# Optimization experiments

Measured on AMD Instinct MI355X. Metric: run time of the kernel, lower is better.

Reference implementation:

```python
import jax, jax.numpy as jnp
import numpy as np

DIM, STATE, EXPAND = 1024, 16, 2
INNER = DIM * EXPAND  # 2048
KSIZE = 4
BATCH, SEQ = 2, 2048


def setup_inputs() -> dict:
    key = jax.random.key(0)
    ks = jax.random.split(key, 7)
    s = 0.02
    return {
        "x": jax.random.normal(ks[0], (BATCH, SEQ, DIM), jnp.float32),
        "W_in": jax.random.normal(ks[1], (2 * INNER, DIM), jnp.float32) * s,
        "conv_w": jax.random.normal(ks[2], (INNER, 1, KSIZE), jnp.float32) * s,
        "conv_b": jnp.zeros((INNER,), jnp.float32),
        "W_x": jax.random.normal(ks[3], (2 * STATE + 1, INNER), jnp.float32) * s,
        "W_dt": jax.random.normal(ks[4], (INNER, STATE), jnp.float32) * s,
        "b_dt": jnp.zeros((INNER,), jnp.float32),
        "W_out": jax.random.normal(ks[5], (DIM, INNER), jnp.float32) * s,
        "A_log": jnp.log(jnp.broadcast_to(
            jnp.arange(1, STATE + 1, dtype=jnp.float32), (INNER, STATE))),
    }


def reference(x, W_in, conv_w, conv_b, W_x, W_dt, b_dt, W_out, A_log):
    b, n, _ = x.shape
    xr = x @ W_in.T                                  # [b,n,2*inner]
    u, res = jnp.split(xr, 2, axis=-1)               # each [b,n,inner]

    # Depthwise conv1d. Original uses padding=3 on both sides but the scan
    # loop only consumes the first n timesteps, which equals a causal conv
    # with left padding KSIZE-1.
    uc = jnp.transpose(u, (0, 2, 1))                 # [b,inner,n]
    uc = jax.lax.conv_general_dilated(
        uc, conv_w, window_strides=(1,), padding=[(KSIZE - 1, 0)],
        dimension_numbers=("NCH", "OIH", "NCH"), feature_group_count=INNER)
    u = jnp.transpose(uc + conv_b[None, :, None], (0, 2, 1))  # [b,n,inner]

    ssm = u @ W_x.T                                  # [b,n,2*state+1]
    dt_in = ssm[..., :STATE]                         # [b,n,state]
    B = ssm[..., STATE:2 * STATE]                    # [b,n,state]
    C = ssm[..., -1]                                 # [b,n]  (scalar readout per step)
    delta = jax.nn.softplus(dt_in @ W_dt.T + b_dt)   # [b,n,inner]
    A = -jnp.exp(A_log)                              # [inner,state]

    def step(h, ts):
        d_t, u_t, b_t, c_t = ts                      # [b,inner],[b,inner],[b,state],[b]
        h = h * jnp.exp(d_t[:, :, None] * A) + u_t[:, :, None] * b_t[:, None, :]
        y = jnp.sum(h, axis=-1) * c_t[:, None]       # y = (h @ C), C scalar
        return h, y

    h0 = jnp.zeros((b, INNER, STATE), x.dtype)
    xs = (jnp.moveaxis(delta, 1, 0), jnp.moveaxis(u, 1, 0),
          jnp.moveaxis(B, 1, 0), jnp.moveaxis(C, 1, 0))
    _, ys = jax.lax.scan(step, h0, xs)               # ys: [n,b,inner]
    y = jnp.moveaxis(ys, 0, 1)                       # [b,n,inner]

    y = y * jax.nn.silu(res)
    return y @ W_out.T                               # [b,n,dim]
```

## Files before the change

### kernel.cpp

```cpp
#include <hip/hip_runtime.h>
#include <math.h>

#define SEQL   2048
#define DIMM   1024
#define NST    16
#define INR    2048
#define TOKS   4096
#define LCH    256
#define NCH    8
#define WARM   64

typedef _Float16 f16;
typedef _Float16 f16x8 __attribute__((ext_vector_type(8)));
typedef float    f32x4 __attribute__((ext_vector_type(4)));

__device__ __forceinline__ int swz(int r) { return (r & 3) ^ ((r >> 2) & 3); }

#define GLDS(SRC, DST) __builtin_amdgcn_global_load_lds( \
    (const __attribute__((address_space(1))) void*)(SRC), \
    (__attribute__((address_space(3))) void*)(DST), 16, 0, 0)

__device__ __forceinline__ void cvt8hi(const float* __restrict__ in, int i,
                                       f16* __restrict__ hi)
{
    const float4* p = (const float4*)(in + (size_t)i * 8);
    float4 a = p[0], b = p[1];
    float v[8] = {a.x, a.y, a.z, a.w, b.x, b.y, b.z, b.w};
    f16x8 H;
    #pragma unroll
    for (int j = 0; j < 8; ++j) H[j] = (f16)v[j];
    *(f16x8*)(hi + (size_t)i * 8) = H;
}

__global__ __launch_bounds__(256) void k_prep(
        const float* __restrict__ Wx,   float* __restrict__ WxT,
        const float* __restrict__ x,    f16* __restrict__ Xhi,
        const float* __restrict__ Win,  f16* __restrict__ Whi,
        const float* __restrict__ Wout, f16* __restrict__ WoH)
{
    const int b = blockIdx.x, tid = threadIdx.x;
    if (b < 264) {
        int i = b * 256 + tid;
        int j = i / INR, ch = i % INR;
        WxT[ch * 33 + j] = Wx[i];
    } else if (b < 264 + 2048) {
        cvt8hi(x, (b - 264) * 256 + tid, Xhi);
    } else if (b < 264 + 4096) {
        cvt8hi(Win, (b - 264 - 2048) * 256 + tid, Whi);
    } else {
        cvt8hi(Wout, (b - 264 - 4096) * 256 + tid, WoH);
    }
}

template<int BN>
__global__ __launch_bounds__(256, 4) void k_gemm(
        const f16* __restrict__ Ah, const f16* __restrict__ Bh,
        int Kloop, int Kstride, int epi, int Nst,
        float* __restrict__ out0, float* __restrict__ out1)
{
    __shared__ alignas(16) f16 SM[8192 + BN * 64];

    const int tid = threadIdx.x;
    const int l   = tid & 63;
    const int w   = tid >> 6;
    const int wm  = (w >> 1) * 64;
    const int wn  = (w & 1) * (BN / 2);
    const int lr  = l & 15;
    const int kg  = l >> 4;
    const int NF  = BN / 32;

    const int wg = blockIdx.x, xcd = wg & 7, pos = wg >> 3;
    int bx, by, kz;
    if (epi) {
        by = (xcd >> 2) * 16 + (pos >> 3);
        bx = (xcd & 3) * 8 + (pos & 7);
        kz = 0;
    } else {
        kz = xcd >> 2;
        by = pos >> 2;
        bx = (xcd & 3) * 4 + (pos & 3);
    }
    const int m0 = by * 128;
    const int n0 = bx * BN;
    const int koff = kz * Kloop;

    const int srow = l >> 2;
    const int sc   = (l & 3) ^ swz(srow);
    const int fo   = lr * 32 + (kg ^ swz(lr)) * 8;

    f32x4 acc[4][4];
    #pragma unroll
    for (int mi = 0; mi < 4; ++mi)
        #pragma unroll
        for (int ni = 0; ni < NF; ++ni)
            acc[mi][ni] = (f32x4){0.f, 0.f, 0.f, 0.f};

    for (int k0 = 0; k0 < Kloop; k0 += 64) {
        __syncthreads();
        #pragma unroll
        for (int hh = 0; hh < 2; ++hh) {
            #pragma unroll
            for (int q = 0; q < 2; ++q) {
                const int rl = w * 32 + q * 16 + srow;
                const size_t go =
                    (size_t)(m0 + rl) * Kstride + koff + k0 + hh * 32 + sc * 8;
                GLDS(Ah + go, &SM[hh * 4096 + (w * 32 + q * 16) * 32]);
            }
            #pragma unroll
            for (int q = 0; q < BN / 64; ++q) {
                const int rl = w * (BN / 4) + q * 16 + srow;
                const size_t go =
                    (size_t)(n0 + rl) * Kstride + koff + k0 + hh * 32 + sc * 8;
                GLDS(Bh + go,
                     &SM[8192 + hh * (BN * 32) + (w * (BN / 4) + q * 16) * 32]);
            }
        }
        __syncthreads();

        #pragma unroll
        for (int hh = 0; hh < 2; ++hh) {
            f16x8 a_[4], b_[4];
            #pragma unroll
            for (int mi = 0; mi < 4; ++mi)
                a_[mi] = *(const f16x8*)&SM[hh * 4096 + (wm + mi * 16) * 32 + fo];
            #pragma unroll
            for (int ni = 0; ni < NF; ++ni)
                b_[ni] = *(const f16x8*)
                    &SM[8192 + hh * (BN * 32) + (wn + ni * 16) * 32 + fo];
            #pragma unroll
            for (int mi = 0; mi < 4; ++mi)
                #pragma unroll
                for (int ni = 0; ni < NF; ++ni)
                    acc[mi][ni] = __builtin_amdgcn_mfma_f32_16x16x32_f16(
                                      a_[mi], b_[ni], acc[mi][ni], 0, 0, 0);
        }
    }

    const int r0 = (l >> 4) * 4;
    float* dst0 = out0 + (epi ? 0 : (size_t)kz * 4194304);
    #pragma unroll
    for (int mi = 0; mi < 4; ++mi)
        #pragma unroll
        for (int ni = 0; ni < NF; ++ni) {
            const int col = n0 + wn + ni * 16 + (l & 15);
            #pragma unroll
            for (int rr = 0; rr < 4; ++rr) {
                const int row = m0 + wm + mi * 16 + r0 + rr;
                float v = acc[mi][ni][rr];
                if (epi) {
                    if (col < INR) {
                        out0[(size_t)row * INR + col] = v;
                    } else {
                        float s = v / (1.f + __expf(-v));
                        out1[(size_t)row * INR + (col - INR)] = s;
                    }
                } else {
                    dst0[(size_t)row * Nst + col] = v;
                }
            }
        }
}

__global__ __launch_bounds__(256) void k_addout(const float* __restrict__ p,
                                                float* __restrict__ out)
{
    int i = blockIdx.x * 256 + threadIdx.x;
    float4 a = ((const float4*)p)[i];
    float4 b = ((const float4*)(p + 4194304))[i];
    float4 o = {a.x + b.x, a.y + b.y, a.z + b.z, a.w + b.w};
    ((float4*)out)[i] = o;
}

__global__ __launch_bounds__(256) void k_conv(const float* __restrict__ u0,
        const float* __restrict__ cw, const float* __restrict__ cb,
        float* __restrict__ uct)
{
    __shared__ float S[67][65];
    const int tid = threadIdx.x;
    const int ch0 = blockIdx.x * 64;
    const int t0  = blockIdx.y * 64;
    const int b   = blockIdx.z;
    const int ci  = tid & 63;
    for (int r = tid >> 6; r < 67; r += 4) {
        int t = t0 - 3 + r;
        S[r][ci] = (t < 0) ? 0.f : u0[((size_t)b*SEQL + t)*INR + ch0 + ci];
    }
    __syncthreads();
    const int ti = tid & 63;
    const int cq = tid >> 6;
    #pragma unroll
    for (int q = 0; q < 16; ++q) {
        int c  = cq + q*4;
        int ch = ch0 + c;
        float w0 = cw[ch*4+0], w1 = cw[ch*4+1], w2 = cw[ch*4+2], w3 = cw[ch*4+3];
        float acc = cb[ch]
            + w0*S[ti+0][c] + w1*S[ti+1][c] + w2*S[ti+2][c] + w3*S[ti+3][c];
        uct[((size_t)b*INR + ch)*SEQL + t0 + ti] = acc;
    }
}

__global__ __launch_bounds__(256) void k_ssm_part(const float* __restrict__ uct,
        const float* __restrict__ WxT, float* __restrict__ part)
{
    const int t  = blockIdx.x * 256 + threadIdx.x;
    const int cs = blockIdx.y;
    const int b  = blockIdx.z;
    const int ch0 = cs * 64;
    float acc[33];
    #pragma unroll
    for (int j = 0; j < 33; ++j) acc[j] = 0.f;
    const float* up = uct + ((size_t)b*INR + ch0)*SEQL + t;
    for (int c = 0; c < 64; ++c) {
        float uv = up[(size_t)c * SEQL];
        const float* wr = WxT + (size_t)(ch0 + c) * 33;
        #pragma unroll
        for (int j = 0; j < 33; ++j) acc[j] = fmaf(uv, wr[j], acc[j]);
    }
    #pragma unroll
    for (int j = 0; j < 33; ++j)
        part[(((size_t)j*32 + cs)*2 + b)*SEQL + t] = acc[j];
}

__global__ __launch_bounds__(256) void k_ssm_reduce(const float* __restrict__ part,
        float* __restrict__ dtin, float* __restrict__ Bm, float* __restrict__ Cv)
{
    int g = blockIdx.x * 256 + threadIdx.x;
    if (g >= 33 * TOKS) return;
    int j = g / TOKS, m = g % TOKS;
    int b = m >> 11, t = m & 2047;
    float s = 0.f;
    #pragma unroll
    for (int cs = 0; cs < 32; ++cs)
        s += part[(((size_t)j*32 + cs)*2 + b)*SEQL + t];
    if (j < 16)      dtin[m*16 + j] = s;
    else if (j < 32) Bm[m*16 + (j-16)] = s;
    else             Cv[m] = s;
}

__global__ __launch_bounds__(256) void k_delta(const float* __restrict__ dtin,
        const float* __restrict__ Wdt, const float* __restrict__ bdt,
        float* __restrict__ dT)
{
    __shared__ float Ds[16][68];
    __shared__ float Ws[16][68];
    const int tid = threadIdx.x;
    const int c0 = blockIdx.x * 64;
    const int m0 = blockIdx.y * 64;
    const int r = tid >> 2, kq = (tid & 3) * 4;
    {
        float4 dv = *(const float4*)&dtin[(size_t)(m0 + r)*16 + kq];
        float4 wv = *(const float4*)&Wdt [(size_t)(c0 + r)*16 + kq];
        Ds[kq+0][r]=dv.x; Ds[kq+1][r]=dv.y; Ds[kq+2][r]=dv.z; Ds[kq+3][r]=dv.w;
        Ws[kq+0][r]=wv.x; Ws[kq+1][r]=wv.y; Ws[kq+2][r]=wv.z; Ws[kq+3][r]=wv.w;
    }
    __syncthreads();
    const int tx = tid & 15, ty = tid >> 4;
    float acc[4][4];
    #pragma unroll
    for (int i = 0; i < 4; ++i)
        #pragma unroll
        for (int j = 0; j < 4; ++j) acc[i][j] = 0.f;
    #pragma unroll
    for (int kk = 0; kk < 16; ++kk) {
        float4 a4 = *(const float4*)&Ds[kk][ty*4];
        float4 b4 = *(const float4*)&Ws[kk][tx*4];
        float a[4] = {a4.x, a4.y, a4.z, a4.w};
        float wv[4] = {b4.x, b4.y, b4.z, b4.w};
        #pragma unroll
        for (int i = 0; i < 4; ++i)
            #pragma unroll
            for (int j = 0; j < 4; ++j)
                acc[i][j] = fmaf(a[i], wv[j], acc[i][j]);
    }
    const int b = m0 >> 11;
    const int tbase = (m0 & 2047) + ty*4;
    #pragma unroll
    for (int j = 0; j < 4; ++j) {
        int ch = c0 + tx*4 + j;
        float bias = bdt[ch];
        float4 o;
        o.x = log1pf(__expf(acc[0][j] + bias));
        o.y = log1pf(__expf(acc[1][j] + bias));
        o.z = log1pf(__expf(acc[2][j] + bias));
        o.w = log1pf(__expf(acc[3][j] + bias));
        *(float4*)&dT[((size_t)b*INR + ch)*SEQL + tbase] = o;
    }
}

__global__ __launch_bounds__(256) void k_scan(const float* __restrict__ dT,
        const float* __restrict__ uct, const float* __restrict__ Bm,
        const float* __restrict__ Cv, const float* __restrict__ Alog,
        const float* __restrict__ sres, f16* __restrict__ AoH)
{
    __shared__ float dS[16][68];
    __shared__ float uS[16][68];
    __shared__ float bT[16][68];
    __shared__ float cS[64];
    __shared__ float hS[16*272];
    const int tid = threadIdx.x;
    const int g = tid >> 4, s = tid & 15;
    const int ch0 = blockIdx.x * 16;
    const int c   = blockIdx.y;
    const int b   = blockIdx.z;
    const int ch  = ch0 + g;
    const int tbase = c * LCH;
    const size_t mb = (size_t)b * SEQL;
    const float A = -__expf(Alog[ch*NST + s]);
    float h = 0.f;
    const int row = tid >> 4, col4 = (tid & 15) * 4;
    const int sB = tid & 15, tq = tid >> 4;
    const int ci = tid & 15, tw = tid >> 4;
    const float* dRow = dT  + ((size_t)b*INR + ch0 + row)*SEQL + tbase;
    const float* uRow = uct + ((size_t)b*INR + ch0 + row)*SEQL + tbase;

    for (int t0 = (c ? -WARM : 0); t0 < LCH; t0 += 64) {
        __syncthreads();
        *(float4*)&dS[row][col4] = *(const float4*)&dRow[t0 + col4];
        *(float4*)&uS[row][col4] = *(const float4*)&uRow[t0 + col4];
        #pragma unroll
        for (int k = 0; k < 4; ++k)
            bT[sB][tq*4 + k] = Bm[(mb + tbase + t0 + tq*4 + k)*16 + sB];
        if (t0 >= 0 && tid < 64) cS[tid] = Cv[mb + tbase + t0 + tid];
        __syncthreads();
        if (t0 < 0) {
            #pragma unroll
            for (int q = 0; q < 16; ++q) {
                float4 d4 = *(const float4*)&dS[g][q*4];
                float4 u4 = *(const float4*)&uS[g][q*4];
                float4 b4 = *(const float4*)&bT[s][q*4];
                h = fmaf(h, __expf(d4.x*A), u4.x*b4.x);
                h = fmaf(h, __expf(d4.y*A), u4.y*b4.y);
                h = fmaf(h, __expf(d4.z*A), u4.z*b4.z);
                h = fmaf(h, __expf(d4.w*A), u4.w*b4.w);
            }
            continue;
        }
        #pragma unroll
        for (int sub = 0; sub < 4; ++sub) {
            #pragma unroll
            for (int q = 0; q < 4; ++q) {
                float4 d4 = *(const float4*)&dS[g][sub*16 + q*4];
                float4 u4 = *(const float4*)&uS[g][sub*16 + q*4];
                float4 b4 = *(const float4*)&bT[s][sub*16 + q*4];
                h = fmaf(h, __expf(d4.x*A), u4.x*b4.x);
                hS[(q*4+0)*272 + g*17 + s] = h;
                h = fmaf(h, __expf(d4.y*A), u4.y*b4.y);
                hS[(q*4+1)*272 + g*17 + s] = h;
                h = fmaf(h, __expf(d4.z*A), u4.z*b4.z);
                hS[(q*4+2)*272 + g*17 + s] = h;
                h = fmaf(h, __expf(d4.w*A), u4.w*b4.w);
                hS[(q*4+3)*272 + g*17 + s] = h;
            }
            __syncthreads();
            float v = 0.f;
            #pragma unroll
            for (int ss = 0; ss < 16; ++ss)
                v += hS[tw*272 + ci*17 + ss];
            const int tl = sub*16 + tw;
            const size_t gi = (mb + tbase + t0 + tl)*INR + ch0 + ci;
            AoH[gi] = (f16)((v * cS[tl]) * sres[gi]);
            __syncthreads();
        }
    }
}

extern "C" void kernel_launch(void* const* d_in, const int* in_sizes, int n_in,
                              void* d_out, int out_size, void* d_ws, size_t ws_size,
                              hipStream_t stream)
{
    (void)in_sizes; (void)n_in; (void)out_size; (void)ws_size;
    const float* x     = (const float*)d_in[0];
    const float* W_in  = (const float*)d_in[1];
    const float* cw    = (const float*)d_in[2];
    const float* cb    = (const float*)d_in[3];
    const float* W_x   = (const float*)d_in[4];
    const float* W_dt  = (const float*)d_in[5];
    const float* b_dt  = (const float*)d_in[6];
    const float* W_out = (const float*)d_in[7];
    const float* A_log = (const float*)d_in[8];
    float* out = (float*)d_out;

    float* ws = (float*)d_ws;
    const size_t MI = 1024 * 1024;
    float* u0   = ws;
    float* sres = ws + 8*MI;
    float* uct  = ws + 16*MI;
    float* part = ws + 24*MI;
    float* dtin = ws + 32*MI;
    float* Bm   = dtin + 65536;
    float* Cv   = Bm + 65536;
    float* WxT  = Cv + 4096;
    float* dT   = u0;
    f16* Xhi = (f16*)(ws + 16*MI);
    f16* Whi = (f16*)(ws + 18*MI);
    f16* AoH = (f16*)(ws + 24*MI);
    f16* WoH = (f16*)(ws + 30*MI);
    float* pK = sres;

    k_prep     <<<dim3(264 + 2048 + 2048 + 1024), 256, 0, stream>>>(
                    W_x, WxT, x, Xhi, W_in, Whi, W_out, WoH);
    k_gemm<128><<<dim3(1024), 256, 0, stream>>>(Xhi, Whi,
                    DIMM, DIMM, 1, INR, u0, sres);
    k_conv     <<<dim3(32, 32, 2), 256, 0, stream>>>(u0, cw, cb, uct);
    k_ssm_part <<<dim3(8, 32, 2), 256, 0, stream>>>(uct, WxT, part);
    k_ssm_reduce<<<dim3((33*TOKS + 255)/256), 256, 0, stream>>>(part, dtin, Bm, Cv);
    k_delta    <<<dim3(32, 64), 256, 0, stream>>>(dtin, W_dt, b_dt, dT);
    k_scan     <<<dim3(128, NCH, 2), 256, 0, stream>>>(dT, uct, Bm, Cv, A_log,
                    sres, AoH);
    k_gemm<64> <<<dim3(1024), 256, 0, stream>>>(AoH, WoH,
                    DIMM, INR, 0, DIMM, pK, nullptr);
    k_addout   <<<dim3(4096), 256, 0, stream>>>(pK, out);
}
```

Baseline: 225.3 us.

## Store conv output and scan partial states in fp16; widen output GEMM tile

The depthwise conv output is stored as fp16 instead of fp32, which halves the traffic for the SSM projection and scan kernels that read it. The scan's shared-memory state buffer becomes fp16, reducing LDS footprint. Separately, the output projection GEMM switches to a 128-wide N tile with half the workgroups and a remapped block index. The cost is lower precision in u and in the partial-state sums.

```diff
diff --git a/kernel.cpp b/kernel.cpp
--- a/kernel.cpp
+++ b/kernel.cpp
@@ -12,6 +12,7 @@
 
 typedef _Float16 f16;
 typedef _Float16 f16x8 __attribute__((ext_vector_type(8)));
+typedef _Float16 f16x4v __attribute__((ext_vector_type(4)));
 typedef float    f32x4 __attribute__((ext_vector_type(4)));
 
 __device__ __forceinline__ int swz(int r) { return (r & 3) ^ ((r >> 2) & 3); }
@@ -77,8 +78,8 @@
         kz = 0;
     } else {
         kz = xcd >> 2;
-        by = pos >> 2;
-        bx = (xcd & 3) * 4 + (pos & 3);
+        by = pos >> 1;
+        bx = (xcd & 3) * 2 + (pos & 1);
     }
     const int m0 = by * 128;
     const int n0 = bx * BN;
@@ -173,7 +174,7 @@
 
 __global__ __launch_bounds__(256) void k_conv(const float* __restrict__ u0,
         const float* __restrict__ cw, const float* __restrict__ cb,
-        float* __restrict__ uct)
+        f16* __restrict__ uct)
 {
     __shared__ float S[67][65];
     const int tid = threadIdx.x;
@@ -195,11 +196,11 @@
         float w0 = cw[ch*4+0], w1 = cw[ch*4+1], w2 = cw[ch*4+2], w3 = cw[ch*4+3];
         float acc = cb[ch]
             + w0*S[ti+0][c] + w1*S[ti+1][c] + w2*S[ti+2][c] + w3*S[ti+3][c];
-        uct[((size_t)b*INR + ch)*SEQL + t0 + ti] = acc;
-    }
-}
-
-__global__ __launch_bounds__(256) void k_ssm_part(const float* __restrict__ uct,
+        uct[((size_t)b*INR + ch)*SEQL + t0 + ti] = (f16)acc;
+    }
+}
+
+__global__ __launch_bounds__(256) void k_ssm_part(const f16* __restrict__ uct,
         const float* __restrict__ WxT, float* __restrict__ part)
 {
     const int t  = blockIdx.x * 256 + threadIdx.x;
@@ -209,9 +210,9 @@
     float acc[33];
     #pragma unroll
     for (int j = 0; j < 33; ++j) acc[j] = 0.f;
-    const float* up = uct + ((size_t)b*INR + ch0)*SEQL + t;
+    const f16* up = uct + ((size_t)b*INR + ch0)*SEQL + t;
     for (int c = 0; c < 64; ++c) {
-        float uv = up[(size_t)c * SEQL];
+        float uv = (float)up[(size_t)c * SEQL];
         const float* wr = WxT + (size_t)(ch0 + c) * 33;
         #pragma unroll
         for (int j = 0; j < 33; ++j) acc[j] = fmaf(uv, wr[j], acc[j]);
@@ -288,7 +289,7 @@
 }
 
 __global__ __launch_bounds__(256) void k_scan(const float* __restrict__ dT,
-        const float* __restrict__ uct, const float* __restrict__ Bm,
+        const f16* __restrict__ uct, const float* __restrict__ Bm,
         const float* __restrict__ Cv, const float* __restrict__ Alog,
         const float* __restrict__ sres, f16* __restrict__ AoH)
 {
@@ -296,7 +297,7 @@
     __shared__ float uS[16][68];
     __shared__ float bT[16][68];
     __shared__ float cS[64];
-    __shared__ float hS[16*272];
+    __shared__ f16 hS[16*272];
     const int tid = threadIdx.x;
     const int g = tid >> 4, s = tid & 15;
     const int ch0 = blockIdx.x * 16;
@@ -311,12 +312,18 @@
     const int sB = tid & 15, tq = tid >> 4;
     const int ci = tid & 15, tw = tid >> 4;
     const float* dRow = dT  + ((size_t)b*INR + ch0 + row)*SEQL + tbase;
-    const float* uRow = uct + ((size_t)b*INR + ch0 + row)*SEQL + tbase;
+    const f16*   uRow = uct + ((size_t)b*INR + ch0 + row)*SEQL + tbase;
 
     for (int t0 = (c ? -WARM : 0); t0 < LCH; t0 += 64) {
         __syncthreads();
         *(float4*)&dS[row][col4] = *(const float4*)&dRow[t0 + col4];
-        *(float4*)&uS[row][col4] = *(const float4*)&uRow[t0 + col4];
+        {
+            f16x4v uv = *(const f16x4v*)&uRow[t0 + col4];
+            uS[row][col4+0] = (float)uv[0];
+            uS[row][col4+1] = (float)uv[1];
+            uS[row][col4+2] = (float)uv[2];
+            uS[row][col4+3] = (float)uv[3];
+        }
         #pragma unroll
         for (int k = 0; k < 4; ++k)
             bT[sB][tq*4 + k] = Bm[(mb + tbase + t0 + tq*4 + k)*16 + sB];
@@ -343,19 +350,19 @@
                 float4 u4 = *(const float4*)&uS[g][sub*16 + q*4];
                 float4 b4 = *(const float4*)&bT[s][sub*16 + q*4];
                 h = fmaf(h, __expf(d4.x*A), u4.x*b4.x);
-                hS[(q*4+0)*272 + g*17 + s] = h;
+                hS[(q*4+0)*272 + g*17 + s] = (f16)h;
                 h = fmaf(h, __expf(d4.y*A), u4.y*b4.y);
-                hS[(q*4+1)*272 + g*17 + s] = h;
+                hS[(q*4+1)*272 + g*17 + s] = (f16)h;
                 h = fmaf(h, __expf(d4.z*A), u4.z*b4.z);
-                hS[(q*4+2)*272 + g*17 + s] = h;
+                hS[(q*4+2)*272 + g*17 + s] = (f16)h;
                 h = fmaf(h, __expf(d4.w*A), u4.w*b4.w);
-                hS[(q*4+3)*272 + g*17 + s] = h;
+                hS[(q*4+3)*272 + g*17 + s] = (f16)h;
             }
             __syncthreads();
             float v = 0.f;
             #pragma unroll
             for (int ss = 0; ss < 16; ++ss)
-                v += hS[tw*272 + ci*17 + ss];
+                v += (float)hS[tw*272 + ci*17 + ss];
             const int tl = sub*16 + tw;
             const size_t gi = (mb + tbase + t0 + tl)*INR + ch0 + ci;
             AoH[gi] = (f16)((v * cS[tl]) * sres[gi]);
@@ -384,7 +391,7 @@
     const size_t MI = 1024 * 1024;
     float* u0   = ws;
     float* sres = ws + 8*MI;
-    float* uct  = ws + 16*MI;
+    f16*   uct  = (f16*)(ws + 16*MI);
     float* part = ws + 24*MI;
     float* dtin = ws + 32*MI;
     float* Bm   = dtin + 65536;
@@ -407,7 +414,7 @@
     k_delta    <<<dim3(32, 64), 256, 0, stream>>>(dtin, W_dt, b_dt, dT);
     k_scan     <<<dim3(128, NCH, 2), 256, 0, stream>>>(dT, uct, Bm, Cv, A_log,
                     sres, AoH);
-    k_gemm<64> <<<dim3(1024), 256, 0, stream>>>(AoH, WoH,
+    k_gemm<128><<<dim3(512), 256, 0, stream>>>(AoH, WoH,
                     DIMM, INR, 0, DIMM, pK, nullptr);
     k_addout   <<<dim3(4096), 256, 0, stream>>>(pK, out);
 }
```

Result: slower. 235.7 us (+4.6%).
